# Optimization experiments

Hardware: AMD Instinct MI355X
Metric: run time of the kernel (lower is better)

The kernel has to match this reference:

```python
import jax, jax.numpy as jnp
import numpy as np

N_SEGMENTS = 1024
D_IN = 16
WIDTH = 128
LATENT = 128
DOT = 64
HEADS = 4
N = 500000


def setup_inputs() -> dict:
    key = jax.random.key(0)
    ks = jax.random.split(key, 12)
    he = lambda k, shape: jax.random.normal(k, shape, jnp.float32) * np.sqrt(2.0 / shape[0])
    inputs = jax.random.normal(ks[0], (N, D_IN), jnp.float32)
    segment_ids = jnp.sort(jax.random.randint(ks[1], (N,), 0, N_SEGMENTS))
    lengths = jax.random.randint(ks[2], (N_SEGMENTS,), 0, 1000)
    return {
        "inputs": inputs,
        "segment_ids": segment_ids,
        "lengths": lengths,
        "W0": he(ks[3], (D_IN, WIDTH)), "b0": jnp.zeros((WIDTH,), jnp.float32),
        "W1": he(ks[4], (WIDTH, WIDTH)), "b1": jnp.zeros((WIDTH,), jnp.float32),
        "Wlat": he(ks[5], (WIDTH, LATENT)), "blat": jnp.zeros((LATENT,), jnp.float32),
        "Wrho": he(ks[6], (LATENT, LATENT)), "brho": jnp.zeros((LATENT,), jnp.float32),
        "W_k": he(ks[7], (LATENT + D_IN, DOT * HEADS)),
        # W_q is zero-initialized in the original; use small random for a non-degenerate test
        "W_q": jax.random.normal(ks[8], (HEADS, DOT), jnp.float32) * 0.02,
    }


def reference(inputs, segment_ids, lengths, W0, b0, W1, b1, Wlat, blat, Wrho, brho, W_k, W_q):
    # psi: Dense(width,relu) x n_layers, then Dense(latent,relu)
    h = jax.nn.relu(inputs @ W0 + b0)            # [N, width]
    h = jax.nn.relu(h @ W1 + b1)                 # [N, width]
    enc = jax.nn.relu(h @ Wlat + blat)           # [N, latent]
    # segment mean aggregation
    ones = jnp.ones((enc.shape[0],), enc.dtype)
    counts = jax.ops.segment_sum(ones, segment_ids, num_segments=N_SEGMENTS)
    seg_sum = jax.ops.segment_sum(enc, segment_ids, num_segments=N_SEGMENTS)
    agg = seg_sum / jnp.maximum(counts, 1.0)[:, None]   # [S, latent]
    # rho
    agg = jax.nn.relu(agg @ Wrho + brho)         # [S, latent]
    # scatter back and concat with raw inputs
    combined = jnp.concatenate([inputs, agg[segment_ids]], axis=-1)  # [N, d+latent]
    # keys: [N, heads, dot] (tf.split over last dim == reshape to (heads, dot))
    keys = (combined @ W_k).reshape(-1, HEADS, DOT)
    pre = jnp.einsum('nhd,hd->nh', keys, W_q) / np.sqrt(float(DOT))  # [N, heads]
    # per-head segment softmax (inference: no attention dropout)
    seg_max = jax.ops.segment_max(pre, segment_ids, num_segments=N_SEGMENTS)
    e = jnp.exp(pre - seg_max[segment_ids])
    denom = jax.ops.segment_sum(e, segment_ids, num_segments=N_SEGMENTS)
    attn = e / denom[segment_ids]                # [N, heads]
    return attn
```

## Files before the change

kernel.cpp:

```cpp
#include <hip/hip_runtime.h>

#define NN 500000
#define NSEG 1024
#define MAXE 2048

__global__ void prep_kernel(const int* __restrict__ seg,
                            const float* __restrict__ Wk,
                            const float* __restrict__ Wq,
                            int* __restrict__ starts,
                            float* __restrict__ Vx) {
  int tid = blockIdx.x * blockDim.x + threadIdx.x;
  int stride = gridDim.x * blockDim.x;
  for (int n = tid; n < NN; n += stride) {
    int s = seg[n];
    int sp = (n == 0) ? -1 : seg[n - 1];
    for (int t = sp + 1; t <= s; ++t) starts[t] = n;
    if (n == NN - 1) { for (int t = s + 1; t <= NSEG; ++t) starts[t] = NN; }
  }
  if (tid < 64) {
    int c = tid >> 2, h = tid & 3;
    float a = 0.f;
    for (int d = 0; d < 64; ++d) a = fmaf(Wk[c * 256 + h * 64 + d], Wq[h * 64 + d], a);
    Vx[tid] = a * 0.125f;
  }
}

__launch_bounds__(256, 4)
__global__ void attn_kernel(const float* __restrict__ x,
                            const int* __restrict__ starts,
                            const float* __restrict__ Vx,
                            float* __restrict__ out) {
  __shared__ float4 sPre[MAXE];
  __shared__ float4 sVx4[16];
  __shared__ float red[4][4];
  __shared__ float bc[4];
  __shared__ int rng[2];

  int s = blockIdx.x, t = threadIdx.x;
  if (t < 16) sVx4[t] = ((const float4*)Vx)[t];
  if (t < 2)  rng[t] = starts[s + t];
  __syncthreads();
  int lo = rng[0], hi = rng[1], len = hi - lo;
  if (len <= 0) return;

  int w = t >> 6;

  if (len <= MAXE) {
    float m0 = -1e30f, m1 = -1e30f, m2 = -1e30f, m3 = -1e30f;
    for (int i = t; i < len; i += 256) {
      const float4* xp = (const float4*)(x + (size_t)(lo + i) * 16);
      float4 a0 = xp[0], a1 = xp[1], a2 = xp[2], a3 = xp[3];
      float xv[16] = {a0.x,a0.y,a0.z,a0.w, a1.x,a1.y,a1.z,a1.w,
                      a2.x,a2.y,a2.z,a2.w, a3.x,a3.y,a3.z,a3.w};
      float p0 = 0.f, p1 = 0.f, p2 = 0.f, p3 = 0.f;
#pragma unroll
      for (int k = 0; k < 16; ++k) {
        float4 vh = sVx4[k];
        p0 = fmaf(xv[k], vh.x, p0);
        p1 = fmaf(xv[k], vh.y, p1);
        p2 = fmaf(xv[k], vh.z, p2);
        p3 = fmaf(xv[k], vh.w, p3);
      }
      sPre[i] = (float4){p0, p1, p2, p3};
      m0 = fmaxf(m0, p0); m1 = fmaxf(m1, p1);
      m2 = fmaxf(m2, p2); m3 = fmaxf(m3, p3);
    }
    for (int o = 1; o < 64; o <<= 1) {
      m0 = fmaxf(m0, __shfl_xor(m0, o)); m1 = fmaxf(m1, __shfl_xor(m1, o));
      m2 = fmaxf(m2, __shfl_xor(m2, o)); m3 = fmaxf(m3, __shfl_xor(m3, o));
    }
    if ((t & 63) == 0) { red[w][0]=m0; red[w][1]=m1; red[w][2]=m2; red[w][3]=m3; }
    __syncthreads();
    if (t < 4) bc[t] = fmaxf(fmaxf(red[0][t], red[1][t]), fmaxf(red[2][t], red[3][t]));
    __syncthreads();
    float M0 = bc[0], M1 = bc[1], M2 = bc[2], M3 = bc[3];

    float s0 = 0.f, s1 = 0.f, s2 = 0.f, s3 = 0.f;
    for (int i = t; i < len; i += 256) {
      float4 p = sPre[i];
      float4 e = { __expf(p.x - M0), __expf(p.y - M1),
                   __expf(p.z - M2), __expf(p.w - M3) };
      sPre[i] = e;
      s0 += e.x; s1 += e.y; s2 += e.z; s3 += e.w;
    }
    for (int o = 1; o < 64; o <<= 1) {
      s0 += __shfl_xor(s0, o); s1 += __shfl_xor(s1, o);
      s2 += __shfl_xor(s2, o); s3 += __shfl_xor(s3, o);
    }
    __syncthreads();
    if ((t & 63) == 0) { red[w][0]=s0; red[w][1]=s1; red[w][2]=s2; red[w][3]=s3; }
    __syncthreads();
    if (t < 4) bc[t] = 1.f / (red[0][t] + red[1][t] + red[2][t] + red[3][t]);
    __syncthreads();
    float i0 = bc[0], i1 = bc[1], i2 = bc[2], i3 = bc[3];

    for (int i = t; i < len; i += 256) {
      float4 e = sPre[i];
      e.x *= i0; e.y *= i1; e.z *= i2; e.w *= i3;
      *(float4*)(out + (size_t)(lo + i) * 4) = e;
    }
  } else {
    float m0 = -1e30f, m1 = -1e30f, m2 = -1e30f, m3 = -1e30f;
    for (int i = t; i < len; i += 256) {
      const float4* xp = (const float4*)(x + (size_t)(lo + i) * 16);
      float4 a0 = xp[0], a1 = xp[1], a2 = xp[2], a3 = xp[3];
      float xv[16] = {a0.x,a0.y,a0.z,a0.w, a1.x,a1.y,a1.z,a1.w,
                      a2.x,a2.y,a2.z,a2.w, a3.x,a3.y,a3.z,a3.w};
      float p0 = 0.f, p1 = 0.f, p2 = 0.f, p3 = 0.f;
#pragma unroll
      for (int k = 0; k < 16; ++k) {
        float4 vh = sVx4[k];
        p0 = fmaf(xv[k], vh.x, p0);
        p1 = fmaf(xv[k], vh.y, p1);
        p2 = fmaf(xv[k], vh.z, p2);
        p3 = fmaf(xv[k], vh.w, p3);
      }
      *(float4*)(out + (size_t)(lo + i) * 4) = (float4){p0, p1, p2, p3};
      m0 = fmaxf(m0, p0); m1 = fmaxf(m1, p1);
      m2 = fmaxf(m2, p2); m3 = fmaxf(m3, p3);
    }
    for (int o = 1; o < 64; o <<= 1) {
      m0 = fmaxf(m0, __shfl_xor(m0, o)); m1 = fmaxf(m1, __shfl_xor(m1, o));
      m2 = fmaxf(m2, __shfl_xor(m2, o)); m3 = fmaxf(m3, __shfl_xor(m3, o));
    }
    if ((t & 63) == 0) { red[w][0]=m0; red[w][1]=m1; red[w][2]=m2; red[w][3]=m3; }
    __syncthreads();
    if (t < 4) bc[t] = fmaxf(fmaxf(red[0][t], red[1][t]), fmaxf(red[2][t], red[3][t]));
    __syncthreads();
    float M0 = bc[0], M1 = bc[1], M2 = bc[2], M3 = bc[3];

    float s0 = 0.f, s1 = 0.f, s2 = 0.f, s3 = 0.f;
    for (int i = t; i < len; i += 256) {
      float4 p = *(const float4*)(out + (size_t)(lo + i) * 4);
      float4 e = { __expf(p.x - M0), __expf(p.y - M1),
                   __expf(p.z - M2), __expf(p.w - M3) };
      *(float4*)(out + (size_t)(lo + i) * 4) = e;
      s0 += e.x; s1 += e.y; s2 += e.z; s3 += e.w;
    }
    for (int o = 1; o < 64; o <<= 1) {
      s0 += __shfl_xor(s0, o); s1 += __shfl_xor(s1, o);
      s2 += __shfl_xor(s2, o); s3 += __shfl_xor(s3, o);
    }
    __syncthreads();
    if ((t & 63) == 0) { red[w][0]=s0; red[w][1]=s1; red[w][2]=s2; red[w][3]=s3; }
    __syncthreads();
    if (t < 4) bc[t] = 1.f / (red[0][t] + red[1][t] + red[2][t] + red[3][t]);
    __syncthreads();
    float i0 = bc[0], i1 = bc[1], i2 = bc[2], i3 = bc[3];

    for (int i = t; i < len; i += 256) {
      float4 e = *(const float4*)(out + (size_t)(lo + i) * 4);
      e.x *= i0; e.y *= i1; e.z *= i2; e.w *= i3;
      *(float4*)(out + (size_t)(lo + i) * 4) = e;
    }
  }
}

extern "C" void kernel_launch(void* const* d_in, const int* in_sizes, int n_in,
                              void* d_out, int out_size, void* d_ws, size_t ws_size,
                              hipStream_t stream) {
  const float* x   = (const float*)d_in[0];
  const int*   seg = (const int*)  d_in[1];
  const float* Wk  = (const float*)d_in[11];
  const float* Wq  = (const float*)d_in[12];
  float* out = (float*)d_out;

  int*   starts = (int*)d_ws;
  float* Vx     = (float*)((char*)d_ws + 4352);

  hipLaunchKernelGGL(prep_kernel, dim3(512), dim3(256), 0, stream,
                     seg, Wk, Wq, starts, Vx);
  hipLaunchKernelGGL(attn_kernel, dim3(NSEG), dim3(256), 0, stream,
                     x, starts, Vx, out);
}
```

Measured before the change: 103.2 us.

## Fuse prep into attention kernel via per-block binary search and inline Wk·Wq fold

Removes the separate prep kernel. Each block now finds its segment bounds by binary-searching the sorted segment ids and computes the 16x4 folded Wk·Wq projection itself in shared memory. This saves one kernel launch and the full scan of segment ids, at the cost of redundant per-block work: about 19 dependent global loads for the search and 64 threads each doing a 64-term dot product.

```diff
diff --git a/kernel.cpp b/kernel.cpp
--- a/kernel.cpp
+++ b/kernel.cpp
@@ -4,46 +4,43 @@
 #define NSEG 1024
 #define MAXE 2048
 
-__global__ void prep_kernel(const int* __restrict__ seg,
+__launch_bounds__(256, 4)
+__global__ void attn_kernel(const float* __restrict__ x,
+                            const int* __restrict__ seg,
                             const float* __restrict__ Wk,
                             const float* __restrict__ Wq,
-                            int* __restrict__ starts,
-                            float* __restrict__ Vx) {
-  int tid = blockIdx.x * blockDim.x + threadIdx.x;
-  int stride = gridDim.x * blockDim.x;
-  for (int n = tid; n < NN; n += stride) {
-    int s = seg[n];
-    int sp = (n == 0) ? -1 : seg[n - 1];
-    for (int t = sp + 1; t <= s; ++t) starts[t] = n;
-    if (n == NN - 1) { for (int t = s + 1; t <= NSEG; ++t) starts[t] = NN; }
-  }
-  if (tid < 64) {
-    int c = tid >> 2, h = tid & 3;
-    float a = 0.f;
-    for (int d = 0; d < 64; ++d) a = fmaf(Wk[c * 256 + h * 64 + d], Wq[h * 64 + d], a);
-    Vx[tid] = a * 0.125f;
-  }
-}
-
-__launch_bounds__(256, 4)
-__global__ void attn_kernel(const float* __restrict__ x,
-                            const int* __restrict__ starts,
-                            const float* __restrict__ Vx,
                             float* __restrict__ out) {
   __shared__ float4 sPre[MAXE];
-  __shared__ float4 sVx4[16];
+  __shared__ float sVx[64];
   __shared__ float red[4][4];
   __shared__ float bc[4];
   __shared__ int rng[2];
 
   int s = blockIdx.x, t = threadIdx.x;
-  if (t < 16) sVx4[t] = ((const float4*)Vx)[t];
-  if (t < 2)  rng[t] = starts[s + t];
+
+  if (t < 64) {
+    int c = t >> 2, h = t & 3;
+    float a = 0.f;
+#pragma unroll 8
+    for (int d = 0; d < 64; ++d)
+      a = fmaf(Wk[c * 256 + h * 64 + d], Wq[h * 64 + d], a);
+    sVx[t] = a * 0.125f;
+  }
+  if (t < 2) {
+    int target = s + t;
+    int lo_ = 0, hi_ = NN;
+    while (lo_ < hi_) {
+      int mid = (lo_ + hi_) >> 1;
+      if (seg[mid] < target) lo_ = mid + 1; else hi_ = mid;
+    }
+    rng[t] = lo_;
+  }
   __syncthreads();
+
   int lo = rng[0], hi = rng[1], len = hi - lo;
   if (len <= 0) return;
-
   int w = t >> 6;
+  const float4* sVx4 = (const float4*)sVx;
 
   if (len <= MAXE) {
     float m0 = -1e30f, m1 = -1e30f, m2 = -1e30f, m3 = -1e30f;
@@ -165,11 +162,6 @@
   const float* Wq  = (const float*)d_in[12];
   float* out = (float*)d_out;
 
-  int*   starts = (int*)d_ws;
-  float* Vx     = (float*)((char*)d_ws + 4352);
-
-  hipLaunchKernelGGL(prep_kernel, dim3(512), dim3(256), 0, stream,
-                     seg, Wk, Wq, starts, Vx);
   hipLaunchKernelGGL(attn_kernel, dim3(NSEG), dim3(256), 0, stream,
-                     x, starts, Vx, out);
+                     x, seg, Wk, Wq, out);
 }
```

New measurement: 106.9 us. 3.5% more time.
